# Kernel optimization log

Measured on AMD Instinct MI355X. Metric: run time of the kernel, lower is better.

Reference implementation:

```python
import jax, jax.numpy as jnp
import numpy as np
import math


def setup_inputs() -> dict:
    key = jax.random.key(0)
    kq, kk, kv, km = jax.random.split(key, 4)
    B, Lq, Lk, D = 4, 4096, 4096, 64
    queries = jax.random.normal(kq, (B, Lq, D), dtype=jnp.float32)
    keys = jax.random.normal(kk, (B, Lk, D), dtype=jnp.float32)
    values = jax.random.normal(kv, (B, Lk, D), dtype=jnp.float32)
    masks = jax.random.randint(km, (B, Lk), 0, 2, dtype=jnp.int32)
    return {"queries": queries, "keys": keys, "values": values, "masks": masks}


def reference(queries, keys, values, masks):
    # scale = sqrt(d_k) (self.scale is None)
    d_k = queries.shape[-1]
    scale = math.sqrt(d_k)
    # scores: [B, Lq, Lk]
    scores = jnp.einsum('bqd,bkd->bqk', queries, keys) / jnp.asarray(scale, queries.dtype)
    # key-padding mask [B, Lk] -> broadcast over Lq; masked positions -> -inf
    neg_inf = jnp.asarray(float('-inf'), scores.dtype)
    scores = jnp.where(masks[:, None, :] == 0, neg_inf, scores)
    attn = jax.nn.softmax(scores, axis=-1)  # dropout p=0 -> identity
    return jnp.einsum('bqk,bkd->bqd', attn, values)
```

## Files before the change

### kernel.cpp

```cpp
#include <hip/hip_runtime.h>


#define B_N    4
#define L      4096
#define DH     64
#define TILE_K 64
#define KPAD   72
#define SPLIT  8
#define SLAB   (L / SPLIT)
#define TILES  (SLAB / TILE_K)
#define QSCALE 0.18033688f

typedef unsigned short ushort8_ma __attribute__((ext_vector_type(8), may_alias));
typedef unsigned short ushort4_ma __attribute__((ext_vector_type(4), may_alias));
typedef float          f32x4_ma   __attribute__((ext_vector_type(4), may_alias));
typedef short          short8     __attribute__((ext_vector_type(8)));
typedef float          f32x4      __attribute__((ext_vector_type(4)));

union v8cast { ushort8_ma u; short8 s; };

static __device__ __forceinline__ short8 ld8(const unsigned short* p) {
    v8cast x; x.u = *(const ushort8_ma*)p; return x.s;
}
static __device__ __forceinline__ unsigned short bf16rne(float f) {
    union { float f; unsigned u; } x; x.f = f;
    unsigned r = x.u + 0x7fffu + ((x.u >> 16) & 1u);
    return (unsigned short)(r >> 16);
}
static __device__ __forceinline__ unsigned short bf16fast(float f) {
    union { float f; unsigned u; } x; x.f = f;
    return (unsigned short)((x.u + 0x8000u) >> 16);
}
static __device__ __forceinline__ float bf16tof(unsigned short u) {
    union { unsigned u; float f; } x; x.u = (unsigned)u << 16; return x.f;
}
static __device__ __forceinline__ float fast_exp2(float x) {
    return __builtin_amdgcn_exp2f(x);
}

__global__ __launch_bounds__(256)
void prepass3(const float* __restrict__ Q, const float* __restrict__ K,
              const float* __restrict__ V,
              unsigned short* __restrict__ Qb, unsigned short* __restrict__ Kb,
              unsigned short* __restrict__ Vt)
{
    __shared__ unsigned short t[64][20];
    const int b  = blockIdx.y;
    const int r0 = blockIdx.x * 16;
    const size_t base = ((size_t)b * L + r0) * DH;

    {
        int i = threadIdx.x;
        int row = i >> 4, d0 = (i & 15) * 4;
        size_t off = base + (size_t)row * DH + d0;
        f32x4_ma q = *(const f32x4_ma*)(Q + off);
        f32x4_ma k = *(const f32x4_ma*)(K + off);
        f32x4_ma v = *(const f32x4_ma*)(V + off);
        ushort4_ma qo, ko;
        #pragma unroll
        for (int j = 0; j < 4; ++j) {
            qo[j] = bf16rne(q[j] * QSCALE);
            ko[j] = bf16rne(k[j]);
            t[d0 + j][row] = bf16rne(v[j]);
        }
        *(ushort4_ma*)(Qb + off) = qo;
        *(ushort4_ma*)(Kb + off) = ko;
    }
    __syncthreads();
    {
        int i = threadIdx.x;
        int d = i >> 2, k4 = (i & 3) * 4;
        ushort4_ma vo = { t[d][k4], t[d][k4 + 1], t[d][k4 + 2], t[d][k4 + 3] };
        *(ushort4_ma*)(Vt + ((size_t)b * DH + d) * L + r0 + k4) = vo;
    }
}

__global__ __launch_bounds__(512)
void fa_split(const unsigned short* __restrict__ Qb,
              const unsigned short* __restrict__ Kb,
              const unsigned short* __restrict__ Vt,
              const int*            __restrict__ Mk,
              unsigned short* __restrict__ ACCp, float* __restrict__ Lp)
{
    __shared__ unsigned short Kl[TILE_K * KPAD];
    __shared__ unsigned short Vl[DH * KPAD];
    __shared__ unsigned short Pl[8][16 * KPAD];
    __shared__ int            Ml[TILE_K];

    const int tid  = threadIdx.x;
    const int wave = tid >> 6;
    const int lane = tid & 63;
    const int l16  = lane & 15;
    const int quad = lane >> 4;

    const int b      = blockIdx.y & (B_N - 1);
    const int slab   = blockIdx.y >> 2;
    const int qblock = blockIdx.x * 128;
    const int kbase  = slab * SLAB;

    short8 aQ[2];
    {
        const unsigned short* qp = Qb + ((size_t)b * L + qblock + wave * 16 + l16) * DH;
        #pragma unroll
        for (int kk = 0; kk < 2; ++kk)
            aQ[kk] = ld8(qp + kk * 32 + quad * 8);
    }

    const unsigned short* Kbb = Kb + (size_t)b * L * DH;
    const unsigned short* Vtb = Vt + (size_t)b * DH * L;
    const int*            Mb  = Mk + (size_t)b * L;

    const int r0 = tid >> 3, d0 = (tid & 7) * 8;

    ushort8_ma kr0, vr0;
    int mr;

    kr0 = *(const ushort8_ma*)(Kbb + (size_t)(kbase + r0) * DH + d0);
    vr0 = *(const ushort8_ma*)(Vtb + (size_t)r0 * L + kbase + d0);
    mr  = Mb[kbase + (tid & 63)];
    *(ushort8_ma*)(&Kl[r0 * KPAD + d0]) = kr0;
    *(ushort8_ma*)(&Vl[r0 * KPAD + d0]) = vr0;
    if (tid < TILE_K) Ml[tid] = mr;
    __syncthreads();

    f32x4 acc_o[4];
    float rs[4] = {0.f, 0.f, 0.f, 0.f};
    const f32x4 zero4 = {0.f, 0.f, 0.f, 0.f};
    #pragma unroll
    for (int n = 0; n < 4; ++n) acc_o[n] = zero4;

    unsigned short* pw = &Pl[wave][0];

    for (int t = 0; t < TILES; ++t) {
        if (t < TILES - 1) {
            const int k0n = kbase + (t + 1) * TILE_K;
            kr0 = *(const ushort8_ma*)(Kbb + (size_t)(k0n + r0) * DH + d0);
            vr0 = *(const ushort8_ma*)(Vtb + (size_t)r0 * L + k0n + d0);
            mr  = Mb[k0n + (tid & 63)];
        }

        f32x4 s[4];
        #pragma unroll
        for (int n = 0; n < 4; ++n) {
            f32x4 acc = zero4;
            #pragma unroll
            for (int kk = 0; kk < 2; ++kk) {
                short8 bK = ld8(&Kl[(n * 16 + l16) * KPAD + kk * 32 + quad * 8]);
                acc = __builtin_amdgcn_mfma_f32_16x16x32_bf16(aQ[kk], bK, acc, 0, 0, 0);
            }
            s[n] = acc;
        }

        float bias[4];
        #pragma unroll
        for (int n = 0; n < 4; ++n) bias[n] = (Ml[n * 16 + l16] == 0) ? -1e30f : 0.f;
        #pragma unroll
        for (int n = 0; n < 4; ++n)
            #pragma unroll
            for (int r = 0; r < 4; ++r) {
                float p = fast_exp2(s[n][r] + bias[n]);
                rs[r] += p;
                pw[(quad * 4 + r) * KPAD + n * 16 + l16] = bf16fast(p);
            }

        #pragma unroll
        for (int kk = 0; kk < 2; ++kk) {
            short8 aP = ld8(&pw[l16 * KPAD + kk * 32 + quad * 8]);
            #pragma unroll
            for (int n = 0; n < 4; ++n) {
                short8 bV = ld8(&Vl[(n * 16 + l16) * KPAD + kk * 32 + quad * 8]);
                acc_o[n] = __builtin_amdgcn_mfma_f32_16x16x32_bf16(aP, bV, acc_o[n], 0, 0, 0);
            }
        }

        __syncthreads();
        if (t < TILES - 1) {
            *(ushort8_ma*)(&Kl[r0 * KPAD + d0]) = kr0;
            *(ushort8_ma*)(&Vl[r0 * KPAD + d0]) = vr0;
            if (tid < TILE_K) Ml[tid] = mr;
            __syncthreads();
        }
    }

    const size_t pbase = ((size_t)(slab * B_N + b)) * L;
    #pragma unroll
    for (int r = 0; r < 4; ++r) {
        float t0 = rs[r];
        t0 += __shfl_xor(t0, 1);
        t0 += __shfl_xor(t0, 2);
        t0 += __shfl_xor(t0, 4);
        t0 += __shfl_xor(t0, 8);
        int qrow = qblock + wave * 16 + quad * 4 + r;
        unsigned short* ap = ACCp + (pbase + qrow) * DH;
        #pragma unroll
        for (int n = 0; n < 4; ++n)
            ap[n * 16 + l16] = bf16rne(acc_o[n][r]);
        if (l16 == 0) Lp[pbase + qrow] = t0;
    }
}

__global__ __launch_bounds__(256)
void fa_combine(const unsigned short* __restrict__ ACCp,
                const float* __restrict__ Lp, float* __restrict__ O)
{
    const int b    = blockIdx.y;
    const int qrow = blockIdx.x * 4 + (threadIdx.x >> 6);
    const int d    = threadIdx.x & 63;

    float lsum = 0.f, o = 0.f;
    #pragma unroll
    for (int s = 0; s < SPLIT; ++s) {
        lsum += Lp[((size_t)(s * B_N + b)) * L + qrow];
        o    += bf16tof(ACCp[(((size_t)(s * B_N + b)) * L + qrow) * DH + d]);
    }
    O[((size_t)b * L + qrow) * DH + d] = o / fmaxf(lsum, 1e-20f);
}

#define TK  64
#define RW  4
#define RB  16
#define KST 67

__global__ __launch_bounds__(256)
void fa_scalar(const float* __restrict__ Q, const float* __restrict__ K,
               const float* __restrict__ V, const int* __restrict__ Mk,
               float* __restrict__ O)
{
    __shared__ float Kt[TK][KST];
    __shared__ float Vts[DH][KST];
    __shared__ float Qs[RB][DH];
    __shared__ float Ps[4][RW][TK];
    __shared__ float Bs[TK];

    const int tid = threadIdx.x, w = tid >> 6, lane = tid & 63;
    const int b = blockIdx.y, row0 = blockIdx.x * RB;

    for (int i = tid; i < RB * DH; i += 256) {
        int r = i >> 6, d = i & 63;
        Qs[r][d] = Q[((size_t)b * L + row0 + r) * DH + d];
    }
    float m[RW], l[RW], acc[RW];
    #pragma unroll
    for (int rr = 0; rr < RW; ++rr) { m[rr] = -1e30f; l[rr] = 0.f; acc[rr] = 0.f; }

    for (int k0 = 0; k0 < L; k0 += TK) {
        __syncthreads();
        for (int i = tid; i < TK * DH; i += 256) {
            int key = i >> 6, d = i & 63;
            Kt[key][d]  = K[((size_t)b * L + k0 + key) * DH + d];
            Vts[d][key] = V[((size_t)b * L + k0 + key) * DH + d];
        }
        if (tid < TK) Bs[tid] = (Mk[(size_t)b * L + k0 + tid] == 0) ? -1e30f : 0.f;
        __syncthreads();
        float s[RW];
        #pragma unroll
        for (int rr = 0; rr < RW; ++rr) s[rr] = 0.f;
        for (int d4 = 0; d4 < DH; d4 += 4) {
            float kv[4];
            #pragma unroll
            for (int j = 0; j < 4; ++j) kv[j] = Kt[lane][d4 + j];
            #pragma unroll
            for (int rr = 0; rr < RW; ++rr)
                #pragma unroll
                for (int j = 0; j < 4; ++j)
                    s[rr] += Qs[w * RW + rr][d4 + j] * kv[j];
        }
        float alpha[RW];
        #pragma unroll
        for (int rr = 0; rr < RW; ++rr) {
            float sv = s[rr] * 0.125f + Bs[lane];
            float t = sv;
            #pragma unroll
            for (int off = 1; off < 64; off <<= 1) t = fmaxf(t, __shfl_xor(t, off));
            float mnew = fmaxf(m[rr], t);
            alpha[rr] = __expf(fminf(m[rr] - mnew, 0.f));
            float p = __expf(fminf(sv - mnew, 0.f));
            Ps[w][rr][lane] = p;
            float su = p;
            #pragma unroll
            for (int off = 1; off < 64; off <<= 1) su += __shfl_xor(su, off);
            l[rr] = l[rr] * alpha[rr] + su;
            m[rr] = mnew;
        }
        __syncthreads();
        #pragma unroll
        for (int rr = 0; rr < RW; ++rr) acc[rr] *= alpha[rr];
        for (int k4 = 0; k4 < TK; k4 += 4) {
            float vv[4];
            #pragma unroll
            for (int j = 0; j < 4; ++j) vv[j] = Vts[lane][k4 + j];
            #pragma unroll
            for (int rr = 0; rr < RW; ++rr)
                #pragma unroll
                for (int j = 0; j < 4; ++j)
                    acc[rr] += Ps[w][rr][k4 + j] * vv[j];
        }
    }
    #pragma unroll
    for (int rr = 0; rr < RW; ++rr) {
        int row = row0 + w * RW + rr;
        O[((size_t)b * L + row) * DH + lane] = acc[rr] / fmaxf(l[rr], 1e-20f);
    }
}

extern "C" void kernel_launch(void* const* d_in, const int* in_sizes, int n_in,
                              void* d_out, int out_size, void* d_ws, size_t ws_size,
                              hipStream_t stream) {
    const float* Q = (const float*)d_in[0];
    const float* K = (const float*)d_in[1];
    const float* V = (const float*)d_in[2];
    const int*   M = (const int*)d_in[3];
    float*       O = (float*)d_out;

    const size_t elems     = (size_t)B_N * L * DH;
    const size_t bf16_need = elems * 2 * 3;
    const size_t acc_elems = (size_t)SPLIT * B_N * L * DH;
    const size_t ml_elems  = (size_t)SPLIT * B_N * L;
    const size_t full_need = bf16_need + acc_elems * 2 + ml_elems * 4;

    unsigned short* Qb = (unsigned short*)d_ws;
    unsigned short* Kb = Qb + elems;
    unsigned short* Vt = Kb + elems;

    if (ws_size >= full_need) {
        unsigned short* ACCp = Vt + elems;
        float*          Lp   = (float*)(ACCp + acc_elems);

        prepass3<<<dim3(L / 16, B_N), dim3(256), 0, stream>>>(Q, K, V, Qb, Kb, Vt);
        fa_split<<<dim3(L / 128, B_N * SPLIT), dim3(512), 0, stream>>>(
            Qb, Kb, Vt, M, ACCp, Lp);
        fa_combine<<<dim3(L / 4, B_N), dim3(256), 0, stream>>>(ACCp, Lp, O);
    } else {
        fa_scalar<<<dim3(L / RB, B_N), dim3(256), 0, stream>>>(Q, K, V, M, O);
    }
}
```

Baseline: 109.7 us.

## Switch split attention kernel to 32x32x16 MFMA with 4 waves per block

Rewrites the split-K attention kernel so each of 4 waves handles 32 query rows using 32x32x16 bf16 MFMA instead of 8 waves of 16 rows with 16x16x32 MFMA. Each thread now loads two K/V chunks per tile, and the P staging buffer, row-sum reduction and output writes are remapped to the 32x32 accumulator layout. The aim is fewer MFMA issues and LDS B-operand reads per unit of work, and better reuse of each K/V tile. The cost is higher register pressure from 16-wide accumulators and row sums, and fewer threads to hide the global loads.

```diff
diff --git a/kernel.cpp b/kernel.cpp
--- a/kernel.cpp
+++ b/kernel.cpp
@@ -15,7 +15,7 @@
 typedef unsigned short ushort4_ma __attribute__((ext_vector_type(4), may_alias));
 typedef float          f32x4_ma   __attribute__((ext_vector_type(4), may_alias));
 typedef short          short8     __attribute__((ext_vector_type(8)));
-typedef float          f32x4      __attribute__((ext_vector_type(4)));
+typedef float          f32x16     __attribute__((ext_vector_type(16)));
 
 union v8cast { ushort8_ma u; short8 s; };
 
@@ -75,59 +75,64 @@
     }
 }
 
-__global__ __launch_bounds__(512)
-void fa_split(const unsigned short* __restrict__ Qb,
-              const unsigned short* __restrict__ Kb,
-              const unsigned short* __restrict__ Vt,
-              const int*            __restrict__ Mk,
-              unsigned short* __restrict__ ACCp, float* __restrict__ Lp)
+__global__ __launch_bounds__(256, 4)
+void fa_split32(const unsigned short* __restrict__ Qb,
+                const unsigned short* __restrict__ Kb,
+                const unsigned short* __restrict__ Vt,
+                const int*            __restrict__ Mk,
+                unsigned short* __restrict__ ACCp, float* __restrict__ Lp)
 {
     __shared__ unsigned short Kl[TILE_K * KPAD];
     __shared__ unsigned short Vl[DH * KPAD];
-    __shared__ unsigned short Pl[8][16 * KPAD];
+    __shared__ unsigned short Pl[4][32 * KPAD];
     __shared__ int            Ml[TILE_K];
 
     const int tid  = threadIdx.x;
     const int wave = tid >> 6;
     const int lane = tid & 63;
-    const int l16  = lane & 15;
-    const int quad = lane >> 4;
+    const int l32  = lane & 31;
+    const int hw   = lane >> 5;
 
     const int b      = blockIdx.y & (B_N - 1);
     const int slab   = blockIdx.y >> 2;
     const int qblock = blockIdx.x * 128;
     const int kbase  = slab * SLAB;
 
-    short8 aQ[2];
+    short8 aQ[4];
     {
-        const unsigned short* qp = Qb + ((size_t)b * L + qblock + wave * 16 + l16) * DH;
-        #pragma unroll
-        for (int kk = 0; kk < 2; ++kk)
-            aQ[kk] = ld8(qp + kk * 32 + quad * 8);
+        const unsigned short* qp = Qb + ((size_t)b * L + qblock + wave * 32 + l32) * DH;
+        #pragma unroll
+        for (int kk = 0; kk < 4; ++kk)
+            aQ[kk] = ld8(qp + kk * 16 + hw * 8);
     }
 
     const unsigned short* Kbb = Kb + (size_t)b * L * DH;
     const unsigned short* Vtb = Vt + (size_t)b * DH * L;
     const int*            Mb  = Mk + (size_t)b * L;
 
+    const int c1 = tid + 256;
     const int r0 = tid >> 3, d0 = (tid & 7) * 8;
-
-    ushort8_ma kr0, vr0;
+    const int r1 = c1 >> 3,  d1 = (c1 & 7) * 8;
+
+    ushort8_ma kr0, kr1, vr0, vr1;
     int mr;
 
     kr0 = *(const ushort8_ma*)(Kbb + (size_t)(kbase + r0) * DH + d0);
+    kr1 = *(const ushort8_ma*)(Kbb + (size_t)(kbase + r1) * DH + d1);
     vr0 = *(const ushort8_ma*)(Vtb + (size_t)r0 * L + kbase + d0);
-    mr  = Mb[kbase + (tid & 63)];
+    vr1 = *(const ushort8_ma*)(Vtb + (size_t)r1 * L + kbase + d1);
+    mr  = Mb[kbase + lane];
     *(ushort8_ma*)(&Kl[r0 * KPAD + d0]) = kr0;
+    *(ushort8_ma*)(&Kl[r1 * KPAD + d1]) = kr1;
     *(ushort8_ma*)(&Vl[r0 * KPAD + d0]) = vr0;
-    if (tid < TILE_K) Ml[tid] = mr;
+    *(ushort8_ma*)(&Vl[r1 * KPAD + d1]) = vr1;
+    if (wave == 0) Ml[lane] = mr;
     __syncthreads();
 
-    f32x4 acc_o[4];
-    float rs[4] = {0.f, 0.f, 0.f, 0.f};
-    const f32x4 zero4 = {0.f, 0.f, 0.f, 0.f};
-    #pragma unroll
-    for (int n = 0; n < 4; ++n) acc_o[n] = zero4;
+    f32x16 acc0 = {0}, acc1 = {0};
+    float rs[16];
+    #pragma unroll
+    for (int r = 0; r < 16; ++r) rs[r] = 0.f;
 
     unsigned short* pw = &Pl[wave][0];
 
@@ -135,67 +140,65 @@
         if (t < TILES - 1) {
             const int k0n = kbase + (t + 1) * TILE_K;
             kr0 = *(const ushort8_ma*)(Kbb + (size_t)(k0n + r0) * DH + d0);
+            kr1 = *(const ushort8_ma*)(Kbb + (size_t)(k0n + r1) * DH + d1);
             vr0 = *(const ushort8_ma*)(Vtb + (size_t)r0 * L + k0n + d0);
-            mr  = Mb[k0n + (tid & 63)];
-        }
-
-        f32x4 s[4];
-        #pragma unroll
-        for (int n = 0; n < 4; ++n) {
-            f32x4 acc = zero4;
-            #pragma unroll
-            for (int kk = 0; kk < 2; ++kk) {
-                short8 bK = ld8(&Kl[(n * 16 + l16) * KPAD + kk * 32 + quad * 8]);
-                acc = __builtin_amdgcn_mfma_f32_16x16x32_bf16(aQ[kk], bK, acc, 0, 0, 0);
+            vr1 = *(const ushort8_ma*)(Vtb + (size_t)r1 * L + k0n + d1);
+            mr  = Mb[k0n + lane];
+        }
+
+        #pragma unroll
+        for (int g = 0; g < 2; ++g) {
+            f32x16 s = {0};
+            #pragma unroll
+            for (int kk = 0; kk < 4; ++kk) {
+                short8 bK = ld8(&Kl[(g * 32 + l32) * KPAD + kk * 16 + hw * 8]);
+                s = __builtin_amdgcn_mfma_f32_32x32x16_bf16(aQ[kk], bK, s, 0, 0, 0);
             }
-            s[n] = acc;
-        }
-
-        float bias[4];
-        #pragma unroll
-        for (int n = 0; n < 4; ++n) bias[n] = (Ml[n * 16 + l16] == 0) ? -1e30f : 0.f;
-        #pragma unroll
-        for (int n = 0; n < 4; ++n)
-            #pragma unroll
-            for (int r = 0; r < 4; ++r) {
-                float p = fast_exp2(s[n][r] + bias[n]);
-                rs[r] += p;
-                pw[(quad * 4 + r) * KPAD + n * 16 + l16] = bf16fast(p);
+            float bias = (Ml[g * 32 + l32] == 0) ? -1e30f : 0.f;
+            #pragma unroll
+            for (int reg = 0; reg < 16; ++reg) {
+                float p = fast_exp2(s[reg] + bias);
+                rs[reg] += p;
+                int row = (reg & 3) + 8 * (reg >> 2) + 4 * hw;
+                pw[row * KPAD + g * 32 + l32] = bf16fast(p);
             }
-
-        #pragma unroll
-        for (int kk = 0; kk < 2; ++kk) {
-            short8 aP = ld8(&pw[l16 * KPAD + kk * 32 + quad * 8]);
-            #pragma unroll
-            for (int n = 0; n < 4; ++n) {
-                short8 bV = ld8(&Vl[(n * 16 + l16) * KPAD + kk * 32 + quad * 8]);
-                acc_o[n] = __builtin_amdgcn_mfma_f32_16x16x32_bf16(aP, bV, acc_o[n], 0, 0, 0);
-            }
+        }
+
+        #pragma unroll
+        for (int kk = 0; kk < 4; ++kk) {
+            short8 aP = ld8(&pw[l32 * KPAD + kk * 16 + hw * 8]);
+            short8 bV0 = ld8(&Vl[l32 * KPAD + kk * 16 + hw * 8]);
+            acc0 = __builtin_amdgcn_mfma_f32_32x32x16_bf16(aP, bV0, acc0, 0, 0, 0);
+            short8 bV1 = ld8(&Vl[(32 + l32) * KPAD + kk * 16 + hw * 8]);
+            acc1 = __builtin_amdgcn_mfma_f32_32x32x16_bf16(aP, bV1, acc1, 0, 0, 0);
         }
 
         __syncthreads();
         if (t < TILES - 1) {
             *(ushort8_ma*)(&Kl[r0 * KPAD + d0]) = kr0;
+            *(ushort8_ma*)(&Kl[r1 * KPAD + d1]) = kr1;
             *(ushort8_ma*)(&Vl[r0 * KPAD + d0]) = vr0;
-            if (tid < TILE_K) Ml[tid] = mr;
+            *(ushort8_ma*)(&Vl[r1 * KPAD + d1]) = vr1;
+            if (wave == 0) Ml[lane] = mr;
             __syncthreads();
         }
     }
 
     const size_t pbase = ((size_t)(slab * B_N + b)) * L;
     #pragma unroll
-    for (int r = 0; r < 4; ++r) {
-        float t0 = rs[r];
+    for (int reg = 0; reg < 16; ++reg) {
+        float t0 = rs[reg];
         t0 += __shfl_xor(t0, 1);
         t0 += __shfl_xor(t0, 2);
         t0 += __shfl_xor(t0, 4);
         t0 += __shfl_xor(t0, 8);
-        int qrow = qblock + wave * 16 + quad * 4 + r;
+        t0 += __shfl_xor(t0, 16);
+        int row  = (reg & 3) + 8 * (reg >> 2) + 4 * hw;
+        int qrow = qblock + wave * 32 + row;
         unsigned short* ap = ACCp + (pbase + qrow) * DH;
-        #pragma unroll
-        for (int n = 0; n < 4; ++n)
-            ap[n * 16 + l16] = bf16rne(acc_o[n][r]);
-        if (l16 == 0) Lp[pbase + qrow] = t0;
+        ap[l32]      = bf16rne(acc0[reg]);
+        ap[32 + l32] = bf16rne(acc1[reg]);
+        if (l32 == 0) Lp[pbase + qrow] = t0;
     }
 }
 
@@ -327,7 +330,7 @@
         float*          Lp   = (float*)(ACCp + acc_elems);
 
         prepass3<<<dim3(L / 16, B_N), dim3(256), 0, stream>>>(Q, K, V, Qb, Kb, Vt);
-        fa_split<<<dim3(L / 128, B_N * SPLIT), dim3(512), 0, stream>>>(
+        fa_split32<<<dim3(L / 128, B_N * SPLIT), dim3(256), 0, stream>>>(
             Qb, Kb, Vt, M, ACCp, Lp);
         fa_combine<<<dim3(L / 4, B_N), dim3(256), 0, stream>>>(ACCp, Lp, O);
     } else {
```

Result: no change. 108.3 us (-1.3%).
